# Kernel optimization log

Hardware: AMD Instinct MI355X
Metric: run time of the kernel (lower is better)

## Reference

```python
import jax, jax.numpy as jnp
import numpy as np

B, T, E, NH, NLEV = 16, 2048, 1024, 16, 12
HD = E // NH


def _level_matrix(length):
    # Vectorized version of get_level_index_weak (base=2): levels[t, s] for s < t.
    tt, ss = np.meshgrid(np.arange(length), np.arange(length), indexing='ij')
    t = tt.copy(); s = ss.copy()
    lev = np.zeros((length, length), dtype=np.int32)
    active = tt > ss
    while active.any():
        l = np.floor(np.log2(np.maximum(t, 1))).astype(np.int64)
        v = (1 << l)
        done = active & (s < v)
        lev[done] = (l[done] + 1).astype(np.int32)
        cont = active & ~done
        t = np.where(cont, t - v, t)
        s = np.where(cont, s - v, s)
        active = cont
    return lev  # lev[t,t] = 0 (diagonal uses level 0)


def setup_inputs() -> dict:
    key = jax.random.key(0)
    ks = jax.random.split(key, 12)
    s = 0.02
    inp = {
        'x': jax.random.normal(ks[0], (B, T, E), jnp.float32),
        'Wq': jax.random.normal(ks[1], (E, E), jnp.float32) * s,
        'bq': jnp.zeros((E,), jnp.float32),
        'Wk': jax.random.normal(ks[2], (E, E), jnp.float32) * s,
        'bk': jnp.zeros((E,), jnp.float32),
        'Wv': jax.random.normal(ks[3], (E, E), jnp.float32) * s,
        'bv': jnp.zeros((E,), jnp.float32),
        'A_log': jax.random.normal(ks[4], (T, NH), jnp.float32),
        'A_bias': jnp.zeros((T, NH), jnp.float32),
        'L': jax.random.normal(ks[5], (T, NH, NLEV), jnp.float32),
        'L_bias': jnp.zeros((T, NH, NLEV), jnp.float32),
        'Wo': jax.random.normal(ks[6], (E, E), jnp.float32) * s,
        'bo': jnp.zeros((E,), jnp.float32),
        'levels': jnp.asarray(_level_matrix(T)),
    }
    return inp


def reference(x, Wq, bq, Wk, bk, Wv, bv, A_log, A_bias, L, L_bias, Wo, bo, levels):
    Bn, Tn, En = x.shape
    NHh = A_log.shape[1]
    HDd = En // NHh
    # q/k projections exist in the original forward but are never used by the
    # hierarchical attention; keep only v (q/k are dead code -> omitted).
    v = (x @ Wv.T + bv).reshape(Bn, Tn, NHh, HDd).transpose(0, 2, 1, 3)  # [B,H,T,D]

    # Decay factors: prod(A[s+1:t+1]) == exp(cumsum(logA)[t] - cumsum(logA)[s]).
    A = jax.nn.sigmoid(A_log + A_bias)            # [T, H]
    cs = jnp.cumsum(jnp.log(A), axis=0)           # [T, H]
    decay = jnp.exp(cs[:, None, :] - cs[None, :, :])  # [t, s, H]; diag == 1

    # Hierarchical level weights: G[t, s, h] = (L + L_bias)[t, h, levels[t, s]].
    Le = L + L_bias                               # [T, H, NLEV]
    G = Le[jnp.arange(Tn)[:, None], :, levels]    # [t, s, H]

    causal = jnp.tril(jnp.ones((Tn, Tn), dtype=bool))[:, :, None]
    Hm = jnp.where(causal, G * decay, jnp.zeros((), x.dtype))  # [t, s, H]

    # Original softmaxes the full row (upper triangle is 0, not -inf) -> keep that.
    attn = jax.nn.softmax(Hm, axis=1)             # over source dim s
    out = jnp.einsum('tsh,bhsd->bhtd', attn, v)   # [B,H,T,D]
    out = out.transpose(0, 2, 1, 3).reshape(Bn, Tn, En)
    return out @ Wo.T + bo
```

## Files before the change

### kernel.cpp

```cpp
#include <hip/hip_runtime.h>
#include <stdint.h>

static constexpr int Bn = 16, Tn = 2048, En = 1024, NHn = 16, HDn = 64, NLEVn = 12;

typedef __attribute__((ext_vector_type(8))) short short8;
typedef __attribute__((ext_vector_type(4))) float floatx4;

__device__ __forceinline__ unsigned short f2bf(float f) {
  unsigned int u = __float_as_uint(f);
  u += 0x7fffu + ((u >> 16) & 1u);
  return (unsigned short)(u >> 16);
}
__device__ __forceinline__ float bf2f(unsigned short s) {
  return __uint_as_float(((unsigned int)s) << 16);
}

__device__ __forceinline__ void async16(const unsigned short* g, unsigned short* l) {
  __builtin_amdgcn_global_load_lds(
      (const __attribute__((address_space(1))) unsigned int*)g,
      (__attribute__((address_space(3))) unsigned int*)l, 16, 0, 0);
}

__global__ void k_cvt(const float* __restrict__ in, unsigned short* __restrict__ out, int n4) {
  int i = blockIdx.x * 256 + threadIdx.x;
  if (i < n4) {
    float4 v = ((const float4*)in)[i];
    ushort4 o;
    o.x = f2bf(v.x); o.y = f2bf(v.y); o.z = f2bf(v.z); o.w = f2bf(v.w);
    ((ushort4*)out)[i] = o;
  }
}

__global__ void k_scan(const float* __restrict__ A_log, const float* __restrict__ A_bias,
                       float* __restrict__ cs) {
  int h = blockIdx.x;
  int tid = threadIdx.x;
  __shared__ float part[256];
  float loc[8];
  float run = 0.f;
#pragma unroll
  for (int j = 0; j < 8; j++) {
    int t = tid * 8 + j;
    float x = A_log[t * NHn + h] + A_bias[t * NHn + h];
    float ls = -log1pf(__expf(-x));
    run += ls;
    loc[j] = run;
  }
  part[tid] = run;
  __syncthreads();
  for (int d = 1; d < 256; d <<= 1) {
    float v = (tid >= d) ? part[tid - d] : 0.f;
    __syncthreads();
    part[tid] += v;
    __syncthreads();
  }
  float off = (tid > 0) ? part[tid - 1] : 0.f;
#pragma unroll
  for (int j = 0; j < 8; j++) cs[(tid * 8 + j) * NHn + h] = loc[j] + off;
}

__global__ void k_weights(const float* __restrict__ L, const float* __restrict__ Lb,
                          const int* __restrict__ levels, const float* __restrict__ cs,
                          unsigned short* __restrict__ P, float* __restrict__ denom) {
  int t = blockIdx.x;
  int tid = threadIdx.x;
  __shared__ float Lrow[NHn * NLEVn];
  __shared__ float cst[NHn];
  __shared__ float dsum[NHn];
  if (tid < NHn * NLEVn) Lrow[tid] = L[t * NHn * NLEVn + tid] + Lb[t * NHn * NLEVn + tid];
  if (tid < NHn) { cst[tid] = cs[t * NHn + tid]; dsum[tid] = 0.f; }
  __syncthreads();
  float acc[NHn];
#pragma unroll
  for (int h = 0; h < NHn; h++) acc[h] = 0.f;
  for (int s = tid; s < Tn; s += 256) {
    int lev = levels[(size_t)t * Tn + s];
    bool causal = (s <= t);
    float csr[NHn];
    const float4* c4 = (const float4*)(cs + s * NHn);
#pragma unroll
    for (int q = 0; q < 4; q++) {
      float4 v = c4[q];
      csr[q * 4 + 0] = v.x; csr[q * 4 + 1] = v.y; csr[q * 4 + 2] = v.z; csr[q * 4 + 3] = v.w;
    }
#pragma unroll
    for (int h = 0; h < NHn; h++) {
      float w = 1.f;
      if (causal) {
        float dec = __expf(cst[h] - csr[h]);
        w = __expf(Lrow[h * NLEVn + lev] * dec);
      }
      unsigned short pb = f2bf(w);
      acc[h] += bf2f(pb);
      P[((size_t)h * Tn + t) * Tn + s] = pb;
    }
  }
  int lane = tid & 63;
#pragma unroll
  for (int h = 0; h < NHn; h++) {
    float v = acc[h];
    for (int o = 32; o > 0; o >>= 1) v += __shfl_down(v, o, 64);
    if (lane == 0) atomicAdd(&dsum[h], v);
  }
  __syncthreads();
  if (tid < NHn) denom[(size_t)tid * Tn + t] = dsum[tid];
}

__global__ __launch_bounds__(512)
void k_gemm_v(const unsigned short* __restrict__ A, const unsigned short* __restrict__ Bm,
              const float* __restrict__ bias, unsigned short* __restrict__ vt) {
  __shared__ unsigned short smem[24576];
  unsigned short* As = smem;
  unsigned short* Bs = smem + 16384;
  const int K = 1024;
  int tid = threadIdx.x;
  int wave = tid >> 6, lane = tid & 63;
  int wm = wave >> 1, wn = wave & 1;

  int flat = blockIdx.y * 8 + blockIdx.x;
  int xcd = flat & 7, slot = flat >> 3;
  int strip = xcd * 16 + (slot >> 3);
  int nt = slot & 7;
  int bm = strip * 256, bn = nt * 128;

  floatx4 zero4 = {0.f, 0.f, 0.f, 0.f};
  floatx4 acc[4][4];
#pragma unroll
  for (int i = 0; i < 4; i++)
#pragma unroll
    for (int j = 0; j < 4; j++) acc[i][j] = zero4;

  for (int k0 = 0; k0 < K; k0 += 64) {
    __syncthreads();
#pragma unroll
    for (int j = 0; j < 4; j++) {
      int f = j * 512 + tid;
      int r = f >> 3, c = f & 7;
      int cg = c ^ (r & 7);
      async16(&A[(size_t)(bm + r) * K + k0 + cg * 8], &As[f * 8]);
    }
#pragma unroll
    for (int j = 0; j < 2; j++) {
      int f = j * 512 + tid;
      int r = f >> 3, c = f & 7;
      int cg = c ^ (r & 7);
      async16(&Bm[(size_t)(bn + r) * K + k0 + cg * 8], &Bs[f * 8]);
    }
    __syncthreads();
#pragma unroll
    for (int kk = 0; kk < 2; kk++) {
      short8 af[4], bfr[4];
      int cgk = kk * 4 + (lane >> 4);
#pragma unroll
      for (int i = 0; i < 4; i++) {
        int m = wm * 64 + i * 16 + (lane & 15);
        af[i] = *(const short8*)&As[m * 64 + ((cgk ^ (m & 7)) * 8)];
        int n = wn * 64 + i * 16 + (lane & 15);
        bfr[i] = *(const short8*)&Bs[n * 64 + ((cgk ^ (n & 7)) * 8)];
      }
#pragma unroll
      for (int i = 0; i < 4; i++)
#pragma unroll
        for (int j = 0; j < 4; j++)
          acc[i][j] = __builtin_amdgcn_mfma_f32_16x16x32_bf16(af[i], bfr[j], acc[i][j], 0, 0, 0);
    }
  }

  int b = bm >> 11, t0 = bm & 2047;
  unsigned short* Ct = smem;
  const int S = 264;
#pragma unroll 1
  for (int pass = 0; pass < 2; pass++) {
    __syncthreads();
    if (wn == pass) {
#pragma unroll
      for (int i = 0; i < 4; i++) {
#pragma unroll
        for (int j = 0; j < 4; j++) {
          int colL = j * 16 + (lane & 15);
          float bia = bias[bn + pass * 64 + colL];
          int rowb = wm * 64 + i * 16 + (lane >> 4) * 4;
          ushort4 p;
          p.x = f2bf(acc[i][j][0] + bia);
          p.y = f2bf(acc[i][j][1] + bia);
          p.z = f2bf(acc[i][j][2] + bia);
          p.w = f2bf(acc[i][j][3] + bia);
          *(ushort4*)&Ct[colL * S + rowb] = p;
        }
      }
    }
    __syncthreads();
#pragma unroll
    for (int cc = 0; cc < 4; cc++) {
      int colL = wave * 8 + cc * 2 + (lane >> 5);
      int gc = bn + pass * 64 + colL;
      int h = gc >> 6, d = gc & 63;
      int tt = (lane & 31) * 8;
      short8 v = *(const short8*)&Ct[colL * S + tt];
      *(short8*)&vt[((size_t)((h * Bn + b) * HDn + d)) * Tn + t0 + tt] = v;
    }
  }
}


#define STAGE_A(kt, half, buf)                                                   \
  {                                                                              \
    _Pragma("unroll")                                                            \
    for (int j_ = 0; j_ < 2; j_++) {                                             \
      int f_ = j_ * 512 + tid;                                                   \
      int r_ = f_ >> 3, c_ = f_ & 7;                                             \
      int cg_ = c_ ^ (r_ & 7);                                                   \
      async16(&Ap[(size_t)(bm + (half) * 128 + r_) * K + (kt) * 64 + cg_ * 8],   \
              &smem[(buf) * 32768 + ((half) * 128 + r_) * 64 + c_ * 8]);         \
    }                                                                            \
  }

#define STAGE_B(kt, half, buf)                                                   \
  {                                                                              \
    _Pragma("unroll")                                                            \
    for (int j_ = 0; j_ < 2; j_++) {                                             \
      int f_ = j_ * 512 + tid;                                                   \
      int r_ = f_ >> 3, c_ = f_ & 7;                                             \
      int cg_ = c_ ^ (r_ & 7);                                                   \
      async16(&Bp[(size_t)(bn + (half) * 128 + r_) * K + (kt) * 64 + cg_ * 8],   \
              &smem[(buf) * 32768 + 16384 + ((half) * 128 + r_) * 64 + c_ * 8]); \
    }                                                                            \
  }

#define LOAD_A(buf, Mh)                                                          \
  {                                                                              \
    _Pragma("unroll")                                                            \
    for (int ii_ = 0; ii_ < 4; ii_++) {                                          \
      int m_ = (Mh) * 128 + wm * 64 + ii_ * 16 + (lane & 15);                    \
      _Pragma("unroll")                                                          \
      for (int kk_ = 0; kk_ < 2; kk_++) {                                        \
        int cgk_ = kk_ * 4 + (lane >> 4);                                        \
        aR[ii_][kk_] =                                                           \
            *(const short8*)&smem[(buf) * 32768 + m_ * 64 + ((cgk_ ^ (m_ & 7)) * 8)]; \
      }                                                                          \
    }                                                                            \
  }

#define LOAD_B(buf, Nh)                                                          \
  {                                                                              \
    _Pragma("unroll")                                                            \
    for (int jj_ = 0; jj_ < 2; jj_++) {                                          \
      int n_ = (Nh) * 128 + wn * 32 + jj_ * 16 + (lane & 15);                    \
      _Pragma("unroll")                                                          \
      for (int kk_ = 0; kk_ < 2; kk_++) {                                        \
        int cgk_ = kk_ * 4 + (lane >> 4);                                        \
        bR[jj_][kk_] = *(const short8*)&smem[(buf) * 32768 + 16384 + n_ * 64 +   \
                                             ((cgk_ ^ (n_ & 7)) * 8)];           \
      }                                                                          \
    }                                                                            \
  }

#define MFMA16(Mh, Nh)                                                           \
  {                                                                              \
    __builtin_amdgcn_s_setprio(1);                                               \
    _Pragma("unroll")                                                            \
    for (int kk_ = 0; kk_ < 2; kk_++)                                            \
      _Pragma("unroll")                                                          \
      for (int ii_ = 0; ii_ < 4; ii_++)                                          \
        _Pragma("unroll")                                                        \
        for (int jj_ = 0; jj_ < 2; jj_++)                                        \
          acc[(Mh) * 4 + ii_][(Nh) * 2 + jj_] = __builtin_amdgcn_mfma_f32_16x16x32_bf16( \
              aR[ii_][kk_], bR[jj_][kk_], acc[(Mh) * 4 + ii_][(Nh) * 2 + jj_], 0, 0, 0); \
    __builtin_amdgcn_s_setprio(0);                                               \
  }

#define WAIT6 asm volatile("s_waitcnt vmcnt(6)" ::: "memory")
#define BAR                                                                      \
  {                                                                              \
    asm volatile("" ::: "memory");                                               \
    __builtin_amdgcn_s_barrier();                                                \
    asm volatile("" ::: "memory");                                               \
  }

#define KTILE_BODY(buf, nbuf, tn)                                                \
  {                                                                              \
                                  \
    STAGE_A(tn, 0, nbuf);                                                        \
    WAIT6; BAR;                                                                  \
    LOAD_A(buf, 0);                                                              \
    LOAD_B(buf, 0);                                                              \
    MFMA16(0, 0);                                                                \
    BAR;                                                                         \
                               \
    STAGE_B(tn, 0, nbuf);                                                        \
    WAIT6; BAR;                                                                  \
    LOAD_B(buf, 1);                                                              \
    MFMA16(0, 1);                                                                \
    BAR;                                                                         \
                               \
    STAGE_B(tn, 1, nbuf);                                                        \
    WAIT6; BAR;                                                                  \
    LOAD_A(buf, 1);                                                              \
    MFMA16(1, 1);                                                                \
    BAR;                                                                         \
                            \
    STAGE_A(tn, 1, nbuf);                                                        \
    WAIT6; BAR;                                                                  \
    LOAD_B(buf, 0);                                                              \
    MFMA16(1, 0);                                                                \
    BAR;                                                                         \
  }

__global__ __launch_bounds__(512, 2)
void k_gemm_attn(const unsigned short* __restrict__ P, const unsigned short* __restrict__ vt,
                 const float* __restrict__ denom, unsigned short* __restrict__ outp) {
  __shared__ unsigned short smem[65536];
  const int K = Tn;
  int tid = threadIdx.x;
  int wave = tid >> 6, lane = tid & 63;
  int wm = wave >> 2, wn = wave & 3;

  int flat = blockIdx.y * 8 + blockIdx.x;
  int wg = (flat & 7) * 64 + (flat >> 3);
  int h = wg >> 5;
  int mt = (wg >> 2) & 7, nt = wg & 3;
  int bm = mt * 256, bn = nt * 256;

  const unsigned short* Ap = P + (size_t)h * Tn * Tn;
  const unsigned short* Bp = vt + (size_t)h * (Bn * HDn) * Tn;

  floatx4 zero4 = {0.f, 0.f, 0.f, 0.f};
  floatx4 acc[8][4];
#pragma unroll
  for (int i = 0; i < 8; i++)
#pragma unroll
    for (int j = 0; j < 4; j++) acc[i][j] = zero4;

  short8 aR[4][2], bR[2][2];

  STAGE_A(0, 0, 0);
  STAGE_B(0, 0, 0);
  STAGE_B(0, 1, 0);
  STAGE_A(0, 1, 0);

  const int nk = K / 64;
  for (int t = 0; t < nk; t++) {
    int buf = t & 1, nbuf = buf ^ 1;
    int tn = (t < nk - 1) ? t + 1 : nk - 1;
    KTILE_BODY(buf, nbuf, tn);
  }
  asm volatile("s_waitcnt vmcnt(0)" ::: "memory");

#pragma unroll
  for (int i = 0; i < 8; i++) {
    int rb = bm + (i >> 2) * 128 + wm * 64 + (i & 3) * 16 + (lane >> 4) * 4;
#pragma unroll
    for (int r = 0; r < 4; r++) {
      int row = rb + r;
      float sc = 1.f / denom[(size_t)h * Tn + row];
#pragma unroll
      for (int j = 0; j < 4; j++) {
        int col = bn + (j >> 1) * 128 + wn * 32 + (j & 1) * 16 + (lane & 15);
        int b = col >> 6, d = col & 63;
        outp[((size_t)(b * Tn + row)) * En + h * HDn + d] = f2bf(acc[i][j][r] * sc);
      }
    }
  }
}

__global__ __launch_bounds__(512, 2)
void k_gemm_out(const unsigned short* __restrict__ A, const unsigned short* __restrict__ Bm,
                const float* __restrict__ bias, float* __restrict__ out) {
  __shared__ unsigned short smem[65536];
  const int K = 1024, N = 1024;
  int tid = threadIdx.x;
  int wave = tid >> 6, lane = tid & 63;
  int wm = wave >> 2, wn = wave & 3;

  int flat = blockIdx.y * 8 + blockIdx.x;
  int wg = (flat & 7) * 64 + (flat >> 3);
  int mt = wg >> 2, nt = wg & 3;
  int bm = mt * 256, bn = nt * 256;

  const unsigned short* Ap = A;
  const unsigned short* Bp = Bm;

  floatx4 zero4 = {0.f, 0.f, 0.f, 0.f};
  floatx4 acc[8][4];
#pragma unroll
  for (int i = 0; i < 8; i++)
#pragma unroll
    for (int j = 0; j < 4; j++) acc[i][j] = zero4;

  short8 aR[4][2], bR[2][2];

  STAGE_A(0, 0, 0);
  STAGE_B(0, 0, 0);
  STAGE_B(0, 1, 0);
  STAGE_A(0, 1, 0);

  const int nk = K / 64;
  for (int t = 0; t < nk; t++) {
    int buf = t & 1, nbuf = buf ^ 1;
    int tn = (t < nk - 1) ? t + 1 : nk - 1;
    KTILE_BODY(buf, nbuf, tn);
  }
  asm volatile("s_waitcnt vmcnt(0)" ::: "memory");

#pragma unroll
  for (int i = 0; i < 8; i++) {
    int rb = bm + (i >> 2) * 128 + wm * 64 + (i & 3) * 16 + (lane >> 4) * 4;
#pragma unroll
    for (int r = 0; r < 4; r++) {
      int row = rb + r;
#pragma unroll
      for (int j = 0; j < 4; j++) {
        int col = bn + (j >> 1) * 128 + wn * 32 + (j & 1) * 16 + (lane & 15);
        out[(size_t)row * N + col] = acc[i][j][r] + bias[col];
      }
    }
  }
}

extern "C" void kernel_launch(void* const* d_in, const int* in_sizes, int n_in,
                              void* d_out, int out_size, void* d_ws, size_t ws_size,
                              hipStream_t stream) {
  const float* x      = (const float*)d_in[0];
  const float* Wv     = (const float*)d_in[5];
  const float* bv     = (const float*)d_in[6];
  const float* A_log  = (const float*)d_in[7];
  const float* A_bias = (const float*)d_in[8];
  const float* L      = (const float*)d_in[9];
  const float* Lb     = (const float*)d_in[10];
  const float* Wo     = (const float*)d_in[11];
  const float* bo     = (const float*)d_in[12];
  const int* levels   = (const int*)d_in[13];
  float* out = (float*)d_out;

  char* ws = (char*)d_ws;
  float* cs            = (float*)(ws + 0);
  float* denom         = (float*)(ws + 131072);
  unsigned short* Wvb  = (unsigned short*)(ws + 262144);
  unsigned short* Wob  = (unsigned short*)(ws + 2359296);
  unsigned short* xb   = (unsigned short*)(ws + 4456448);
  unsigned short* Pw   = (unsigned short*)(ws + 4456448);
  unsigned short* vt   = (unsigned short*)(ws + 138674176);
  unsigned short* outp = (unsigned short*)(ws + 205783040);
  if (ws_size < 272891904ULL) return;

  int nx4 = Bn * Tn * En / 4;
  k_cvt<<<(nx4 + 255) / 256, 256, 0, stream>>>(x, xb, nx4);
  int nw4 = En * En / 4;
  k_cvt<<<(nw4 + 255) / 256, 256, 0, stream>>>(Wv, Wvb, nw4);
  k_cvt<<<(nw4 + 255) / 256, 256, 0, stream>>>(Wo, Wob, nw4);
  k_scan<<<NHn, 256, 0, stream>>>(A_log, A_bias, cs);

  k_gemm_v<<<dim3(8, 128), 512, 0, stream>>>(xb, Wvb, bv, vt);

  k_weights<<<Tn, 256, 0, stream>>>(L, Lb, levels, cs, Pw, denom);

  k_gemm_attn<<<dim3(8, 64), 512, 0, stream>>>(Pw, vt, denom, outp);

  k_gemm_out<<<dim3(8, 64), 512, 0, stream>>>(outp, Wob, bo, out);
}
```

Measured before the change: 605.6 us.

## Fuse decay/exp weight computation and row-sum into attention GEMM A-tile staging

```diff
diff --git a/kernel.cpp b/kernel.cpp
--- a/kernel.cpp
+++ b/kernel.cpp
@@ -1,4 +1,5 @@
 #include <hip/hip_runtime.h>
+#include <hip/hip_fp16.h>
 #include <stdint.h>
 
 static constexpr int Bn = 16, Tn = 2048, En = 1024, NHn = 16, HDn = 64, NLEVn = 12;
@@ -32,7 +33,7 @@
 }
 
 __global__ void k_scan(const float* __restrict__ A_log, const float* __restrict__ A_bias,
-                       float* __restrict__ cs) {
+                       float* __restrict__ csT) {
   int h = blockIdx.x;
   int tid = threadIdx.x;
   __shared__ float part[256];
@@ -56,54 +57,24 @@
   }
   float off = (tid > 0) ? part[tid - 1] : 0.f;
 #pragma unroll
-  for (int j = 0; j < 8; j++) cs[(tid * 8 + j) * NHn + h] = loc[j] + off;
-}
-
-__global__ void k_weights(const float* __restrict__ L, const float* __restrict__ Lb,
-                          const int* __restrict__ levels, const float* __restrict__ cs,
-                          unsigned short* __restrict__ P, float* __restrict__ denom) {
+  for (int j = 0; j < 8; j++) csT[(size_t)h * Tn + tid * 8 + j] = loc[j] + off;
+}
+
+__global__ void k_gather(const float* __restrict__ L, const float* __restrict__ Lb,
+                         const int* __restrict__ levels, unsigned short* __restrict__ G) {
   int t = blockIdx.x;
   int tid = threadIdx.x;
   __shared__ float Lrow[NHn * NLEVn];
-  __shared__ float cst[NHn];
-  __shared__ float dsum[NHn];
   if (tid < NHn * NLEVn) Lrow[tid] = L[t * NHn * NLEVn + tid] + Lb[t * NHn * NLEVn + tid];
-  if (tid < NHn) { cst[tid] = cs[t * NHn + tid]; dsum[tid] = 0.f; }
   __syncthreads();
-  float acc[NHn];
-#pragma unroll
-  for (int h = 0; h < NHn; h++) acc[h] = 0.f;
   for (int s = tid; s < Tn; s += 256) {
     int lev = levels[(size_t)t * Tn + s];
-    bool causal = (s <= t);
-    float csr[NHn];
-    const float4* c4 = (const float4*)(cs + s * NHn);
-#pragma unroll
-    for (int q = 0; q < 4; q++) {
-      float4 v = c4[q];
-      csr[q * 4 + 0] = v.x; csr[q * 4 + 1] = v.y; csr[q * 4 + 2] = v.z; csr[q * 4 + 3] = v.w;
-    }
 #pragma unroll
     for (int h = 0; h < NHn; h++) {
-      float w = 1.f;
-      if (causal) {
-        float dec = __expf(cst[h] - csr[h]);
-        w = __expf(Lrow[h * NLEVn + lev] * dec);
-      }
-      unsigned short pb = f2bf(w);
-      acc[h] += bf2f(pb);
-      P[((size_t)h * Tn + t) * Tn + s] = pb;
-    }
-  }
-  int lane = tid & 63;
-#pragma unroll
-  for (int h = 0; h < NHn; h++) {
-    float v = acc[h];
-    for (int o = 32; o > 0; o >>= 1) v += __shfl_down(v, o, 64);
-    if (lane == 0) atomicAdd(&dsum[h], v);
-  }
-  __syncthreads();
-  if (tid < NHn) denom[(size_t)tid * Tn + t] = dsum[tid];
+      __half hv = __float2half(Lrow[h * NLEVn + lev]);
+      G[((size_t)h * Tn + t) * Tn + s] = __half_as_ushort(hv);
+    }
+  }
 }
 
 __global__ __launch_bounds__(512)
@@ -270,6 +241,8 @@
   }
 
 #define WAIT6 asm volatile("s_waitcnt vmcnt(6)" ::: "memory")
+#define WAIT4 asm volatile("s_waitcnt vmcnt(4)" ::: "memory")
+#define LGKM0 asm volatile("s_waitcnt lgkmcnt(0)" ::: "memory")
 #define BAR                                                                      \
   {                                                                              \
     asm volatile("" ::: "memory");                                               \
@@ -277,39 +250,47 @@
     asm volatile("" ::: "memory");                                               \
   }
 
-#define KTILE_BODY(buf, nbuf, tn)                                                \
-  {                                                                              \
-                                  \
-    STAGE_A(tn, 0, nbuf);                                                        \
-    WAIT6; BAR;                                                                  \
-    LOAD_A(buf, 0);                                                              \
-    LOAD_B(buf, 0);                                                              \
-    MFMA16(0, 0);                                                                \
-    BAR;                                                                         \
-                               \
-    STAGE_B(tn, 0, nbuf);                                                        \
-    WAIT6; BAR;                                                                  \
-    LOAD_B(buf, 1);                                                              \
-    MFMA16(0, 1);                                                                \
-    BAR;                                                                         \
-                               \
-    STAGE_B(tn, 1, nbuf);                                                        \
-    WAIT6; BAR;                                                                  \
-    LOAD_A(buf, 1);                                                              \
-    MFMA16(1, 1);                                                                \
-    BAR;                                                                         \
-                            \
-    STAGE_A(tn, 1, nbuf);                                                        \
-    WAIT6; BAR;                                                                  \
-    LOAD_B(buf, 0);                                                              \
-    MFMA16(1, 0);                                                                \
-    BAR;                                                                         \
+#define TRANSFORM(half, buf, kt, cb)                                             \
+  {                                                                              \
+    int cg_ = (tid & 7) ^ ((tid >> 3) & 7);                                      \
+    float4 csA = *(const float4*)&csr_lds[(cb) * 64 + cg_ * 8];                  \
+    float4 csBv = *(const float4*)&csr_lds[(cb) * 64 + cg_ * 8 + 4];             \
+    int sb_ = (kt) * 64 + cg_ * 8;                                               \
+    _Pragma("unroll")                                                            \
+    for (int j_ = 0; j_ < 2; j_++) {                                             \
+      int r_ = (half) * 128 + j_ * 64 + (tid >> 3);                              \
+      int au_ = (buf) * 32768 + r_ * 64 + (tid & 7) * 8;                         \
+      short8 g8 = *(const short8*)&smem[au_];                                    \
+      float cstv = cst_lds[r_];                                                  \
+      int trow_ = bm + r_;                                                       \
+      float sum_ = 0.f;                                                          \
+      short8 o8;                                                                 \
+      _Pragma("unroll")                                                          \
+      for (int e_ = 0; e_ < 8; e_++) {                                           \
+        float w_ = 1.0f;                                                         \
+        if (sb_ + e_ <= trow_) {                                                 \
+          __half hh_ = __ushort_as_half((unsigned short)g8[e_]);                 \
+          float g_ = __half2float(hh_);                                          \
+          float csr_ = (e_ < 4) ? ((const float*)&csA)[e_ & 3]                   \
+                                : ((const float*)&csBv)[e_ & 3];                 \
+          w_ = __expf(g_ * __expf(cstv - csr_));                                 \
+        }                                                                        \
+        unsigned short pb_ = f2bf(w_);                                           \
+        o8[e_] = (short)pb_;                                                     \
+        sum_ += bf2f(pb_);                                                       \
+      }                                                                          \
+      *(short8*)&smem[au_] = o8;                                                 \
+      dsumR[(half) * 2 + j_] += sum_;                                            \
+    }                                                                            \
   }
 
 __global__ __launch_bounds__(512, 2)
-void k_gemm_attn(const unsigned short* __restrict__ P, const unsigned short* __restrict__ vt,
-                 const float* __restrict__ denom, unsigned short* __restrict__ outp) {
+void k_gemm_attn(const unsigned short* __restrict__ G, const unsigned short* __restrict__ vt,
+                 const float* __restrict__ csT, unsigned short* __restrict__ outp) {
   __shared__ unsigned short smem[65536];
+  __shared__ float csr_lds[2 * 64];
+  __shared__ float cst_lds[256];
+  __shared__ float dsum_lds[256];
   const int K = Tn;
   int tid = threadIdx.x;
   int wave = tid >> 6, lane = tid & 63;
@@ -321,8 +302,9 @@
   int mt = (wg >> 2) & 7, nt = wg & 3;
   int bm = mt * 256, bn = nt * 256;
 
-  const unsigned short* Ap = P + (size_t)h * Tn * Tn;
+  const unsigned short* Ap = G + (size_t)h * Tn * Tn;
   const unsigned short* Bp = vt + (size_t)h * (Bn * HDn) * Tn;
+  const float* csh = csT + (size_t)h * Tn;
 
   floatx4 zero4 = {0.f, 0.f, 0.f, 0.f};
   floatx4 acc[8][4];
@@ -332,27 +314,67 @@
     for (int j = 0; j < 4; j++) acc[i][j] = zero4;
 
   short8 aR[4][2], bR[2][2];
-
+  float dsumR[4] = {0.f, 0.f, 0.f, 0.f};
+
+  if (tid < 256) cst_lds[tid] = csh[bm + tid];
+  if (tid < 64) csr_lds[tid] = csh[tid];
   STAGE_A(0, 0, 0);
   STAGE_B(0, 0, 0);
   STAGE_B(0, 1, 0);
   STAGE_A(0, 1, 0);
+  __syncthreads();
+  TRANSFORM(0, 0, 0, 0);
+  LGKM0;
 
   const int nk = K / 64;
   for (int t = 0; t < nk; t++) {
     int buf = t & 1, nbuf = buf ^ 1;
     int tn = (t < nk - 1) ? t + 1 : nk - 1;
-    KTILE_BODY(buf, nbuf, tn);
+
+    if (tid < 64) csr_lds[nbuf * 64 + tid] = csh[tn * 64 + tid];
+    STAGE_A(tn, 0, nbuf);
+    WAIT6; LGKM0; BAR;
+    LOAD_A(buf, 0);
+    LOAD_B(buf, 0);
+    MFMA16(0, 0);
+    BAR;
+    STAGE_B(tn, 0, nbuf);
+    WAIT4; BAR;
+    LOAD_B(buf, 1);
+    MFMA16(0, 1);
+    TRANSFORM(1, buf, t, buf);
+    LGKM0; BAR;
+    STAGE_B(tn, 1, nbuf);
+    WAIT6; BAR;
+    LOAD_A(buf, 1);
+    MFMA16(1, 1);
+    BAR;
+    STAGE_A(tn, 1, nbuf);
+    WAIT6; BAR;
+    LOAD_B(buf, 0);
+    MFMA16(1, 0);
+    if (t < nk - 1) { TRANSFORM(0, nbuf, t + 1, nbuf); }
+    LGKM0; BAR;
   }
   asm volatile("s_waitcnt vmcnt(0)" ::: "memory");
 
 #pragma unroll
+  for (int q = 0; q < 4; q++) {
+    float v = dsumR[q];
+    v += __shfl_xor(v, 1, 64);
+    v += __shfl_xor(v, 2, 64);
+    v += __shfl_xor(v, 4, 64);
+    if ((tid & 7) == 0) dsum_lds[q * 64 + (tid >> 3)] = v;
+  }
+  __syncthreads();
+
+#pragma unroll
   for (int i = 0; i < 8; i++) {
-    int rb = bm + (i >> 2) * 128 + wm * 64 + (i & 3) * 16 + (lane >> 4) * 4;
+    int rl = (i >> 2) * 128 + wm * 64 + (i & 3) * 16 + (lane >> 4) * 4;
 #pragma unroll
     for (int r = 0; r < 4; r++) {
-      int row = rb + r;
-      float sc = 1.f / denom[(size_t)h * Tn + row];
+      int row = bm + rl + r;
+      float sc = 1.f / dsum_lds[rl + r];
 #pragma unroll
       for (int j = 0; j < 4; j++) {
         int col = bn + (j >> 1) * 128 + wn * 32 + (j & 1) * 16 + (lane & 15);
@@ -398,7 +420,27 @@
   for (int t = 0; t < nk; t++) {
     int buf = t & 1, nbuf = buf ^ 1;
     int tn = (t < nk - 1) ? t + 1 : nk - 1;
-    KTILE_BODY(buf, nbuf, tn);
+    STAGE_A(tn, 0, nbuf);
+    WAIT6; BAR;
+    LOAD_A(buf, 0);
+    LOAD_B(buf, 0);
+    MFMA16(0, 0);
+    BAR;
+    STAGE_B(tn, 0, nbuf);
+    WAIT6; BAR;
+    LOAD_B(buf, 1);
+    MFMA16(0, 1);
+    BAR;
+    STAGE_B(tn, 1, nbuf);
+    WAIT6; BAR;
+    LOAD_A(buf, 1);
+    MFMA16(1, 1);
+    BAR;
+    STAGE_A(tn, 1, nbuf);
+    WAIT6; BAR;
+    LOAD_B(buf, 0);
+    MFMA16(1, 0);
+    BAR;
   }
   asm volatile("s_waitcnt vmcnt(0)" ::: "memory");
 
@@ -433,12 +475,11 @@
   float* out = (float*)d_out;
 
   char* ws = (char*)d_ws;
-  float* cs            = (float*)(ws + 0);
-  float* denom         = (float*)(ws + 131072);
+  float* csT           = (float*)(ws + 0);
   unsigned short* Wvb  = (unsigned short*)(ws + 262144);
   unsigned short* Wob  = (unsigned short*)(ws + 2359296);
   unsigned short* xb   = (unsigned short*)(ws + 4456448);
-  unsigned short* Pw   = (unsigned short*)(ws + 4456448);
+  unsigned short* Gw   = (unsigned short*)(ws + 4456448);
   unsigned short* vt   = (unsigned short*)(ws + 138674176);
   unsigned short* outp = (unsigned short*)(ws + 205783040);
   if (ws_size < 272891904ULL) return;
@@ -448,13 +489,13 @@
   int nw4 = En * En / 4;
   k_cvt<<<(nw4 + 255) / 256, 256, 0, stream>>>(Wv, Wvb, nw4);
   k_cvt<<<(nw4 + 255) / 256, 256, 0, stream>>>(Wo, Wob, nw4);
-  k_scan<<<NHn, 256, 0, stream>>>(A_log, A_bias, cs);
+  k_scan<<<NHn, 256, 0, stream>>>(A_log, A_bias, csT);
 
   k_gemm_v<<<dim3(8, 128), 512, 0, stream>>>(xb, Wvb, bv, vt);
 
-  k_weights<<<Tn, 256, 0, stream>>>(L, Lb, levels, cs, Pw, denom);
-
-  k_gemm_attn<<<dim3(8, 64), 512, 0, stream>>>(Pw, vt, denom, outp);
+  k_gather<<<Tn, 256, 0, stream>>>(L, Lb, levels, Gw);
+
+  k_gemm_attn<<<dim3(8, 64), 512, 0, stream>>>(Gw, vt, csT, outp);
 
   k_gemm_out<<<dim3(8, 64), 512, 0, stream>>>(outp, Wob, bo, out);
 }
```

Result: slower. 706.2 us (+16.6%).
